# Optimization experiments

Hardware: AMD Instinct MI355X
Metric: run time of the kernel (lower is better)

Reference implementation:

```python
import jax, jax.numpy as jnp
import numpy as np

B, T, S, L, R, H, UE = 64, 256, 16, 128, 16, 256, 64


def setup_inputs() -> dict:
    key = jax.random.key(0)
    ks = jax.random.split(key, 10)
    u = jax.random.normal(ks[0], (B, T, UE), jnp.float32)
    k = 0.1 * jax.random.normal(ks[1], (B, T, L), jnp.float32)
    K = 0.1 * jax.random.normal(ks[2], (B, T, L, R), jnp.float32)
    eps_z = jax.random.normal(ks[3], (T, S, B, L), jnp.float32)
    eps_w = jax.random.normal(ks[4], (T, S, B, R), jnp.float32)
    W1 = jax.random.normal(ks[5], (L, H), jnp.float32) / np.sqrt(L).astype(np.float32)
    W2 = jax.random.normal(ks[6], (H, L), jnp.float32) / np.sqrt(H).astype(np.float32)
    m_init = jax.random.normal(ks[7], (L,), jnp.float32)
    Q_diag = jax.random.uniform(ks[8], (L,), jnp.float32, 0.1, 1.0)
    Q0_diag = jax.random.uniform(ks[9], (L,), jnp.float32, 0.5, 1.5)
    return dict(u=u, k=k, K=K, eps_z=eps_z, eps_w=eps_w, W1=W1, W2=W2,
                m_init=m_init, Q_diag=Q_diag, Q0_diag=Q0_diag, n_samples=S)


def reference(u, k, K, eps_z, eps_w, W1, W2, m_init, Q_diag, Q0_diag, n_samples):
    Bn, Tn, Ln, Rn = K.shape
    ue = u.shape[-1]
    I_r = jnp.eye(Rn, dtype=K.dtype)

    def bmv(A, x):      # A: [B,L,R], x: [...,B,R] -> [...,B,L]
        return jnp.einsum('blr,...br->...bl', A, x)

    def bmvT(A, x):     # A: [B,L,R], x: [...,B,L] -> [...,B,R]
        return jnp.einsum('blr,...bl->...br', A, x)

    def mean_fn(z):
        return z + jnp.tanh(z @ W1) @ W2

    def step_core(m, K_t, k_t, ez, ew, q_a):
        # A = I + K^T diag(q_a) K  (rank x rank)
        A = I_r + jnp.einsum('blr,l,blq->brq', K_t, q_a, K_t)
        Lc = jnp.linalg.cholesky(A)
        Linv = jax.scipy.linalg.solve_triangular(
            Lc, jnp.broadcast_to(I_r, Lc.shape), lower=True)

        def csolve(x):  # solve A y = x via Linv^T Linv x
            y = jnp.einsum('bij,...bj->...bi', Linv, x)
            return jnp.einsum('bji,...bj->...bi', Linv, y)

        # gain direction; inner shift always uses Q_diag (as in torch source)
        g = k_t - bmv(K_t, csolve(bmvT(K_t, m + Q_diag * k_t)))
        m_f = m + q_a * g
        z_p = jnp.sqrt(q_a) * ez
        z_f = m_f + z_p - bmv(K_t, csolve(bmvT(K_t, z_p) + ew))
        qp = jnp.sum(q_a * g * g, axis=-1)
        M = A - I_r  # = K^T diag(q_a) K
        tr = -jnp.einsum('bij,bjk,bik->b', Linv, M, Linv)
        logdet = 2.0 * jnp.sum(jnp.log(jnp.diagonal(Lc, axis1=-2, axis2=-1)), axis=-1)
        kl = 0.5 * (qp + tr + logdet)
        return z_f, m_f, z_p, kl

    # ---- t = 0 (uses initial covariance Q0_diag) ----
    m0 = jnp.broadcast_to(m_init, (Bn, Ln))
    m0 = m0.at[:, :ue].add(u[:, 0])
    z_f0, m_f0, z_p0, kl0 = step_core(m0, K[:, 0], k[:, 0], eps_z[0], eps_w[0], Q0_diag)

    # ---- t = 1..T-1: sequential nonlinear filter scan ----
    def scan_fn(z_prev, xs):
        u_t, k_t, K_t, ez, ew = xs
        m = mean_fn(z_prev)            # [S,B,L]
        m = m.at[..., :ue].add(u_t)    # broadcast input over samples
        z_f, m_f, z_p, kl = step_core(m, K_t, k_t, ez, ew, Q_diag)
        return z_f, (z_f, m_f.mean(axis=0), z_p, kl.mean(axis=0))

    xs = (jnp.swapaxes(u[:, 1:], 0, 1),
          jnp.swapaxes(k[:, 1:], 0, 1),
          jnp.swapaxes(K[:, 1:], 0, 1),
          eps_z[1:], eps_w[1:])
    _, (z_fs, m_fs, z_ps, kls) = jax.lax.scan(scan_fn, z_f0, xs)

    z_f = jnp.transpose(jnp.concatenate([z_f0[None], z_fs], 0), (1, 2, 0, 3))  # [S,B,T,L]
    m_f = jnp.transpose(jnp.concatenate([m_f0[None], m_fs], 0), (1, 0, 2))     # [B,T,L]
    z_p = jnp.transpose(jnp.concatenate([z_p0[None], z_ps], 0), (1, 2, 0, 3))  # [S,B,T,L]
    kl = jnp.concatenate([kl0[None], kls], 0).T                                 # [B,T]
    return z_f, m_f, z_p, kl
```

## Files before the change

kernel.cpp:

```cpp
#include <hip/hip_runtime.h>
#include <cstddef>

typedef _Float16 half8 __attribute__((ext_vector_type(8)));
typedef _Float16 half4 __attribute__((ext_vector_type(4)));
typedef float f32x4 __attribute__((ext_vector_type(4)));

#define MFMA32(A, B, C) __builtin_amdgcn_mfma_f32_16x16x32_f16(A, B, C, 0, 0, 0)
#define MFMA16(A, B, C) __builtin_amdgcn_mfma_f32_16x16x16f16(A, B, C, 0, 0, 0)

__global__ void kbp_kernel(const float* __restrict__ Kg,
                           const float* __restrict__ kg,
                           const float* __restrict__ Qd,
                           const float* __restrict__ Q0d,
                           float* __restrict__ Ainv,
                           float* __restrict__ klc,
                           float* __restrict__ Pg,
                           float* __restrict__ cg,
                           _Float16* __restrict__ Kt16) {
  int bt = blockIdx.x;
  int t = bt & 255;
  int tid = threadIdx.x;
  __shared__ float Ks[128][17];
  __shared__ float qs[128], qgl[128], kv[128];
  __shared__ float A[16][17];
  __shared__ float Lm[16][17];
  __shared__ float Li[16][17];
  __shared__ float Ai[16][17];
  __shared__ float Ps[128][17];
  __shared__ float yp[16][17];
  __shared__ float yv[16];
  __shared__ float logdet_s;

  const float* kp = Kg + (size_t)bt * 2048;
  for (int i = tid; i < 2048; i += 256) Ks[i >> 4][i & 15] = kp[i];
  if (tid < 128) {
    qs[tid] = (t == 0) ? Q0d[tid] : Qd[tid];
    qgl[tid] = Qd[tid];
    kv[tid] = kg[(size_t)bt * 128 + tid];
  }
  __syncthreads();
  {
    int r = tid >> 4, cc = tid & 15;
    float acc = (r == cc) ? 1.0f : 0.0f;
    for (int l = 0; l < 128; ++l) acc += Ks[l][r] * qs[l] * Ks[l][cc];
    A[r][cc] = acc;
  }
  __syncthreads();
  if (tid == 0) {
    float ld = 0.f;
    for (int j = 0; j < 16; ++j) {
      float d = A[j][j];
      for (int p = 0; p < j; ++p) d -= Lm[j][p] * Lm[j][p];
      d = sqrtf(d);
      Lm[j][j] = d;
      ld += logf(d);
      float inv = 1.0f / d;
      for (int i = j + 1; i < 16; ++i) {
        float s = A[i][j];
        for (int p = 0; p < j; ++p) s -= Lm[i][p] * Lm[j][p];
        Lm[i][j] = s * inv;
      }
    }
    logdet_s = 2.0f * ld;
  }
  __syncthreads();
  if (tid < 16) {
    int cc = tid;
    for (int i = 0; i < 16; ++i) {
      if (i < cc) { Li[i][cc] = 0.f; continue; }
      float s = (i == cc) ? 1.0f : 0.0f;
      for (int p = cc; p < i; ++p) s -= Lm[i][p] * Li[p][cc];
      Li[i][cc] = s / Lm[i][i];
    }
  }
  __syncthreads();
  {
    int r = tid >> 4, cc = tid & 15;
    float s = 0.f;
    for (int i = 0; i < 16; ++i) s += Li[i][r] * Li[i][cc];
    Ai[r][cc] = s;
    Ainv[(size_t)bt * 256 + tid] = s;
  }
  {
    int r = tid & 15, seg = tid >> 4;
    float s = 0.f;
    for (int l = seg * 8; l < seg * 8 + 8; ++l) s += Ks[l][r] * qgl[l] * kv[l];
    yp[seg][r] = s;
  }
  __syncthreads();
  if (tid < 16) {
    float s = 0.f;
    for (int sg = 0; sg < 16; ++sg) s += yp[sg][tid];
    yv[tid] = s;
  }
  if (tid == 0) {
    float trace = 0.f;
    for (int i = 0; i < 16; ++i) trace += Ai[i][i];
    klc[bt] = 0.5f * (trace - 16.0f + logdet_s);
  }
  {
    int l = tid >> 1, r0 = (tid & 1) * 8;
    float q = qs[l];
    float pr[8];
    for (int r = 0; r < 8; ++r) {
      float s = 0.f;
      for (int j = 0; j < 16; ++j) s += Ks[l][j] * Ai[j][r0 + r];
      pr[r] = q * s;
      Ps[l][r0 + r] = pr[r];
    }
    float* pd = Pg + (size_t)bt * 2048 + l * 16 + r0;
    f32x4 v0 = {pr[0], pr[1], pr[2], pr[3]};
    f32x4 v1 = {pr[4], pr[5], pr[6], pr[7]};
    *(f32x4*)pd = v0;
    *(f32x4*)(pd + 4) = v1;
  }
  __syncthreads();
  if (tid < 128) {
    int l = tid;
    float s = qs[l] * kv[l];
    for (int r = 0; r < 16; ++r) s -= Ps[l][r] * yv[r];
    cg[(size_t)bt * 128 + l] = s;
  }
  {
    int r = tid >> 4, l0 = (tid & 15) * 8;
    half8 v;
    for (int j = 0; j < 8; ++j) v[j] = (_Float16)Ks[l0 + j][r];
    *(half8*)(Kt16 + (size_t)bt * 2048 + r * 128 + l0) = v;
  }
}

__global__ void kc_kernel(const float* __restrict__ Kg,
                          const float* __restrict__ epsz,
                          const float* __restrict__ epsw,
                          const float* __restrict__ Qd,
                          const float* __restrict__ Q0d,
                          const float* __restrict__ Ainv,
                          float* __restrict__ out_zf,
                          float* __restrict__ out_zp,
                          int wzp) {
  int idx = blockIdx.x;
  int t = idx >> 6, b = idx & 63;
  int bt = b * 256 + t;
  __shared__ float Ks[128][16];
  __shared__ float Ai[16][16];
  __shared__ float zp[16][129];
  __shared__ float hh[16][17];
  __shared__ float ww[16][17];
  __shared__ float sq[128];
  const float* kp = Kg + (size_t)bt * 2048;
  for (int i = threadIdx.x; i < 2048; i += 256) ((float*)Ks)[i] = kp[i];
  ((float*)Ai)[threadIdx.x] = Ainv[(size_t)bt * 256 + threadIdx.x];
  const float* q = (t == 0) ? Q0d : Qd;
  if (threadIdx.x < 128) sq[threadIdx.x] = sqrtf(q[threadIdx.x]);
  __syncthreads();
  for (int i = threadIdx.x; i < 2048; i += 256) {
    int s = i >> 7, l = i & 127;
    float v = sq[l] * epsz[(((size_t)t * 16 + s) * 64 + b) * 128 + l];
    zp[s][l] = v;
    if (wzp) out_zp[(((size_t)s * 64 + b) * 256 + t) * 128 + l] = v;
  }
  __syncthreads();
  {
    int s = threadIdx.x >> 4, r = threadIdx.x & 15;
    float acc = epsw[(((size_t)t * 16 + s) * 64 + b) * 16 + r];
    for (int l = 0; l < 128; ++l) acc += Ks[l][r] * zp[s][l];
    hh[s][r] = acc;
  }
  __syncthreads();
  {
    int s = threadIdx.x >> 4, r = threadIdx.x & 15;
    float acc = 0.f;
    for (int j = 0; j < 16; ++j) acc += Ai[r][j] * hh[s][j];
    ww[s][r] = acc;
  }
  __syncthreads();
  for (int i = threadIdx.x; i < 2048; i += 256) {
    int s = i >> 7, l = i & 127;
    float acc = 0.f;
    for (int r = 0; r < 16; ++r) acc += Ks[l][r] * ww[s][r];
    out_zf[(((size_t)s * 64 + b) * 256 + t) * 128 + l] = zp[s][l] - acc;
  }
}

__global__ void kzp_kernel(const float* __restrict__ epsz,
                           const float* __restrict__ Qd,
                           const float* __restrict__ Q0d,
                           float* __restrict__ out_zp) {
  for (size_t i = (size_t)blockIdx.x * blockDim.x + threadIdx.x; i < (size_t)33554432;
       i += (size_t)gridDim.x * blockDim.x) {
    int l = (int)(i & 127);
    int t = (int)((i >> 7) & 255);
    int sb = (int)(i >> 15);
    int s = sb >> 6, b = sb & 63;
    float q = (t == 0) ? Q0d[l] : Qd[l];
    out_zp[i] = sqrtf(q) * epsz[(((size_t)t * 16 + s) * 64 + b) * 128 + l];
  }
}

__launch_bounds__(256, 1)
__global__ void kscan_kernel(const float* __restrict__ ug,
                             const float* __restrict__ W1,
                             const float* __restrict__ W2,
                             const float* __restrict__ m_init,
                             const float* __restrict__ Qd,
                             const float* __restrict__ Q0d,
                             const float* __restrict__ Pg,
                             const float* __restrict__ cg,
                             const _Float16* __restrict__ Kt16,
                             const float* __restrict__ klc,
                             float* __restrict__ out_zf,
                             float* __restrict__ out_mf,
                             float* __restrict__ out_kl) {
  const int b = blockIdx.x;
  const int tid = threadIdx.x;
  const int wv = tid >> 6;
  const int ln = tid & 63;
  const int g = ln >> 4;
  const int c = ln & 15;
  const int swz = (c & 7) << 3;

  __shared__ __align__(16) _Float16 svh[16 * 128];
  __shared__ __align__(16) _Float16 svl[16 * 128];
  __shared__ __align__(16) _Float16 hb[16 * 256];
  __shared__ float h2p[4][16][18];
  __shared__ float qpp[64];

  half8 w1f[4][4];
#pragma unroll
  for (int mt = 0; mt < 4; ++mt)
#pragma unroll
    for (int kt = 0; kt < 4; ++kt) {
      half8 v;
#pragma unroll
      for (int j = 0; j < 8; ++j)
        v[j] = (_Float16)W1[(size_t)(kt * 32 + g * 8 + j) * 256 + (wv * 64 + mt * 16 + c)];
      w1f[mt][kt] = v;
    }
  half8 w2f[2][8];
#pragma unroll
  for (int mt = 0; mt < 2; ++mt)
#pragma unroll
    for (int kt = 0; kt < 8; ++kt) {
      half8 v;
#pragma unroll
      for (int j = 0; j < 8; ++j)
        v[j] = (_Float16)W2[(size_t)(kt * 32 + g * 8 + j) * 128 + (wv * 32 + mt * 16 + c)];
      w2f[mt][kt] = v;
    }

  f32x4 qivQ[2], qivQ0[2];
#pragma unroll
  for (int mt = 0; mt < 2; ++mt) {
    int base = wv * 32 + mt * 16 + g * 4;
    f32x4 q = *(const f32x4*)&Qd[base];
    f32x4 q0 = *(const f32x4*)&Q0d[base];
#pragma unroll
    for (int r = 0; r < 4; ++r) {
      qivQ[mt][r] = 1.0f / q[r];
      qivQ0[mt][r] = 1.0f / q0[r];
    }
  }

  f32x4 zreg[2];
  f32x4 m[2];
  half4 ktfrag[2];
  f32x4 pA[2];
  f32x4 cvec[2];
  f32x4 zpcv[2];
  f32x4 ureg[2] = {};
  float klcv = 0.f;

  auto STAGE = [&](int t) {
    size_t bt = (size_t)b * 256 + t;
#pragma unroll
    for (int kt = 0; kt < 2; ++kt)
      ktfrag[kt] = *(const half4*)&Kt16[bt * 2048 + (size_t)c * 128 + wv * 32 + kt * 16 + g * 4];
#pragma unroll
    for (int mt = 0; mt < 2; ++mt) {
      pA[mt] = *(const f32x4*)&Pg[bt * 2048 + (size_t)(wv * 32 + mt * 16 + c) * 16 + g * 4];
      cvec[mt] = *(const f32x4*)&cg[bt * 128 + wv * 32 + mt * 16 + g * 4];
      zpcv[mt] = *(const f32x4*)&out_zf[(((size_t)c * 64 + b) * 256 + t) * 128 + wv * 32 + mt * 16 + g * 4];
      if (wv < 2) ureg[mt] = *(const f32x4*)&ug[bt * 64 + wv * 32 + mt * 16 + g * 4];
    }
    if (tid < 16) klcv = klc[bt];
  };

  auto MM3P = [&]() {
    f32x4 h2acc = {};
#pragma unroll
    for (int kt = 0; kt < 2; ++kt) {
      half4 mh, ml;
#pragma unroll
      for (int r = 0; r < 4; ++r) {
        float x = m[kt][r];
        _Float16 h = (_Float16)x;
        mh[r] = h;
        ml[r] = (_Float16)(x - (float)h);
      }
      h2acc = MFMA16(ktfrag[kt], mh, h2acc);
      h2acc = MFMA16(ktfrag[kt], ml, h2acc);
    }
#pragma unroll
    for (int r = 0; r < 4; ++r) h2p[wv][g * 4 + r][c] = h2acc[r];
  };

  auto PHASE_A = [&]() {
    f32x4 acc1[4] = {};
#pragma unroll
    for (int kt = 0; kt < 4; ++kt) {
      half8 zh = *(const half8*)&svh[c * 128 + ((kt * 32 + g * 8) ^ swz)];
      half8 zl = *(const half8*)&svl[c * 128 + ((kt * 32 + g * 8) ^ swz)];
#pragma unroll
      for (int mt = 0; mt < 4; ++mt) {
        acc1[mt] = MFMA32(w1f[mt][kt], zh, acc1[mt]);
        acc1[mt] = MFMA32(w1f[mt][kt], zl, acc1[mt]);
      }
    }
#pragma unroll
    for (int mt = 0; mt < 4; ++mt) {
      half4 th;
#pragma unroll
      for (int r = 0; r < 4; ++r) {
        float x = acc1[mt][r];
        float e = __expf(2.0f * x);
        th[r] = (_Float16)(1.0f - 2.0f / (e + 1.0f));
      }
      *(half4*)&hb[c * 256 + ((wv * 64 + mt * 16 + g * 4) ^ swz)] = th;
    }
  };

  auto PHASE_B = [&]() {
    f32x4 acc2[2] = {};
#pragma unroll
    for (int kt = 0; kt < 8; ++kt) {
      half8 hf = *(const half8*)&hb[c * 256 + ((kt * 32 + g * 8) ^ swz)];
#pragma unroll
      for (int mt = 0; mt < 2; ++mt) acc2[mt] = MFMA32(w2f[mt][kt], hf, acc2[mt]);
    }
#pragma unroll
    for (int mt = 0; mt < 2; ++mt) {
      m[mt] = zreg[mt] + acc2[mt];
      if (wv < 2) m[mt] += ureg[mt];
    }
    MM3P();
  };

  auto PHASE_C = [&](int t, bool q0) {
    float h2[4];
#pragma unroll
    for (int j = 0; j < 4; ++j)
      h2[j] = h2p[0][g * 4 + j][c] + h2p[1][g * 4 + j][c] + h2p[2][g * 4 + j][c] + h2p[3][g * 4 + j][c];
    half4 h2h, h2l;
#pragma unroll
    for (int j = 0; j < 4; ++j) {
      _Float16 h = (_Float16)h2[j];
      h2h[j] = h;
      h2l[j] = (_Float16)(h2[j] - (float)h);
    }
    float qpl = 0.f;
    f32x4 mfv[2];
#pragma unroll
    for (int mt = 0; mt < 2; ++mt) {
      half4 ph, pl;
#pragma unroll
      for (int r = 0; r < 4; ++r) {
        float x = pA[mt][r];
        _Float16 h = (_Float16)x;
        ph[r] = h;
        pl[r] = (_Float16)(x - (float)h);
      }
      f32x4 macc = {};
      macc = MFMA16(ph, h2h, macc);
      macc = MFMA16(ph, h2l, macc);
      macc = MFMA16(pl, h2h, macc);
      f32x4 zf4;
      f32x4 qiv = q0 ? qivQ0[mt] : qivQ[mt];
#pragma unroll
      for (int r = 0; r < 4; ++r) {
        float d = cvec[mt][r] - macc[r];
        float mf = m[mt][r] + d;
        float zf = mf + zpcv[mt][r];
        qpl += d * d * qiv[r];
        zreg[mt][r] = zf;
        zf4[r] = zf;
        mfv[mt][r] = mf;
      }
      *(f32x4*)&out_zf[(((size_t)c * 64 + b) * 256 + t) * 128 + wv * 32 + mt * 16 + g * 4] = zf4;
      half4 zh, zl;
#pragma unroll
      for (int r = 0; r < 4; ++r) {
        _Float16 h = (_Float16)zf4[r];
        zh[r] = h;
        zl[r] = (_Float16)(zf4[r] - (float)h);
      }
      *(half4*)&svh[c * 128 + ((wv * 32 + mt * 16 + g * 4) ^ swz)] = zh;
      *(half4*)&svl[c * 128 + ((wv * 32 + mt * 16 + g * 4) ^ swz)] = zl;
    }
#pragma unroll
    for (int mt = 0; mt < 2; ++mt) {
      f32x4 v = mfv[mt];
#pragma unroll
      for (int r = 0; r < 4; ++r) {
        float x = v[r];
        x += __shfl_xor(x, 1);
        x += __shfl_xor(x, 2);
        x += __shfl_xor(x, 4);
        x += __shfl_xor(x, 8);
        v[r] = x * 0.0625f;
      }
      if (c == 0)
        *(f32x4*)&out_mf[((size_t)b * 256 + t) * 128 + wv * 32 + mt * 16 + g * 4] = v;
    }
    {
      float x = qpl;
      x += __shfl_xor(x, 16);
      x += __shfl_xor(x, 32);
      if (g == 0) qpp[wv * 16 + c] = x;
    }
  };

  auto KL_FIN = [&](int t) {
    if (tid < 16) {
      float v = qpp[tid] + qpp[16 + tid] + qpp[32 + tid] + qpp[48 + tid];
      v += __shfl_xor(v, 1);
      v += __shfl_xor(v, 2);
      v += __shfl_xor(v, 4);
      v += __shfl_xor(v, 8);
      if (tid == 0) out_kl[(size_t)b * 256 + t] = 0.03125f * v + klcv;
    }
  };

  STAGE(0);
#pragma unroll
  for (int mt = 0; mt < 2; ++mt) {
    f32x4 mi = *(const f32x4*)&m_init[wv * 32 + mt * 16 + g * 4];
    if (wv < 2) mi += ureg[mt];
    m[mt] = mi;
  }
  MM3P();
  __syncthreads();
  PHASE_C(0, true);
  __syncthreads();
  KL_FIN(0);

  for (int t = 1; t < 256; ++t) {
    STAGE(t);
    PHASE_A();
    __syncthreads();
    PHASE_B();
    __syncthreads();
    PHASE_C(t, false);
    __syncthreads();
    KL_FIN(t);
  }
}

extern "C" void kernel_launch(void* const* d_in, const int* in_sizes, int n_in,
                              void* d_out, int out_size, void* d_ws, size_t ws_size,
                              hipStream_t stream) {
  (void)in_sizes; (void)n_in; (void)out_size;
  const float* u   = (const float*)d_in[0];
  const float* kk  = (const float*)d_in[1];
  const float* Kg  = (const float*)d_in[2];
  const float* epz = (const float*)d_in[3];
  const float* epw = (const float*)d_in[4];
  const float* W1  = (const float*)d_in[5];
  const float* W2  = (const float*)d_in[6];
  const float* mi  = (const float*)d_in[7];
  const float* Qd  = (const float*)d_in[8];
  const float* Q0d = (const float*)d_in[9];

  float* out_zf = (float*)d_out;
  float* out_mf = out_zf + (size_t)33554432;
  float* out_zp = out_mf + (size_t)2097152;
  float* out_kl = out_zp + (size_t)33554432;

  char* ws = (char*)d_ws;
  float* Ainv    = (float*)ws;
  float* klc     = (float*)(ws + 16777216);
  float* cg      = (float*)(ws + 16842752);
  _Float16* Kt16 = (_Float16*)(ws + 25231360);
  const size_t need_full = 226557952;
  bool fb = ws_size < need_full;
  float* Pg = fb ? out_zp : (float*)(ws + 92340224);
  int wzp = fb ? 0 : 1;

  kbp_kernel<<<16384, 256, 0, stream>>>(Kg, kk, Qd, Q0d, Ainv, klc, Pg, cg, Kt16);
  kc_kernel<<<16384, 256, 0, stream>>>(Kg, epz, epw, Qd, Q0d, Ainv, out_zf, out_zp, wzp);
  kscan_kernel<<<64, 256, 0, stream>>>(u, W1, W2, mi, Qd, Q0d, Pg, cg, Kt16, klc,
                                       out_zf, out_mf, out_kl);
  if (fb) kzp_kernel<<<2048, 256, 0, stream>>>(epz, Qd, Q0d, out_zp);
}
```

Baseline: 1.169 ms.

## Precompute K^T W2 products, restructure prep kernel per-wave, double-buffer scan staging

The prep kernel now handles four (b,t) problems per block, one per wavefront. It uses a shuffle-based Cholesky, stores P in fp16 and folds the input u into the constant term c. A new kernel precomputes R = K^T W2 in fp16, so the scan can compute K^T m as K^T z + R tanh(...) in parallel with the W2 matmul. This shortens the serial dependency chain per timestep. The scan loop is unrolled by two with double-buffered register staging of the next step's operands, and the LDS layouts are changed to a rotating swizzle. The cost is an extra precompute pass that writes a large R buffer, plus fp16 rounding of R and P.

```diff
diff --git a/kernel.cpp b/kernel.cpp
--- a/kernel.cpp
+++ b/kernel.cpp
@@ -8,124 +8,182 @@
 #define MFMA32(A, B, C) __builtin_amdgcn_mfma_f32_16x16x32_f16(A, B, C, 0, 0, 0)
 #define MFMA16(A, B, C) __builtin_amdgcn_mfma_f32_16x16x16f16(A, B, C, 0, 0, 0)
 
-__global__ void kbp_kernel(const float* __restrict__ Kg,
-                           const float* __restrict__ kg,
-                           const float* __restrict__ Qd,
-                           const float* __restrict__ Q0d,
-                           float* __restrict__ Ainv,
-                           float* __restrict__ klc,
-                           float* __restrict__ Pg,
-                           float* __restrict__ cg,
-                           _Float16* __restrict__ Kt16) {
-  int bt = blockIdx.x;
-  int t = bt & 255;
+__global__ void kprep1_kernel(const float* __restrict__ Kg,
+                              const float* __restrict__ kg,
+                              const float* __restrict__ ug,
+                              const float* __restrict__ Qd,
+                              const float* __restrict__ Q0d,
+                              float* __restrict__ Ainv,
+                              float* __restrict__ klc,
+                              _Float16* __restrict__ P16,
+                              float* __restrict__ cg) {
   int tid = threadIdx.x;
-  __shared__ float Ks[128][17];
-  __shared__ float qs[128], qgl[128], kv[128];
-  __shared__ float A[16][17];
-  __shared__ float Lm[16][17];
-  __shared__ float Li[16][17];
-  __shared__ float Ai[16][17];
-  __shared__ float Ps[128][17];
-  __shared__ float yp[16][17];
-  __shared__ float yv[16];
-  __shared__ float logdet_s;
-
-  const float* kp = Kg + (size_t)bt * 2048;
-  for (int i = tid; i < 2048; i += 256) Ks[i >> 4][i & 15] = kp[i];
-  if (tid < 128) {
-    qs[tid] = (t == 0) ? Q0d[tid] : Qd[tid];
-    qgl[tid] = Qd[tid];
-    kv[tid] = kg[(size_t)bt * 128 + tid];
-  }
-  __syncthreads();
-  {
-    int r = tid >> 4, cc = tid & 15;
-    float acc = (r == cc) ? 1.0f : 0.0f;
-    for (int l = 0; l < 128; ++l) acc += Ks[l][r] * qs[l] * Ks[l][cc];
-    A[r][cc] = acc;
-  }
-  __syncthreads();
-  if (tid == 0) {
+  int wv = tid >> 6, ln = tid & 63;
+  size_t bt = (size_t)blockIdx.x * 4 + wv;
+  int t = (int)(bt & 255);
+  __shared__ float Ks[4][128][20];
+  __shared__ float qs[4][128];
+  __shared__ float vvs[4][128];
+  __shared__ float Asm[4][16][20];
+  __shared__ float LiL[4][16][20];
+  __shared__ float AiS[4][16][20];
+  __shared__ float yps[4][4][16];
+  __shared__ float yvs[4][16];
+
+  const float* kp = Kg + bt * 2048;
+  for (int i = ln; i < 2048; i += 64) Ks[wv][i >> 4][i & 15] = kp[i];
+  for (int l = ln; l < 128; l += 64) {
+    float q = (t == 0) ? Q0d[l] : Qd[l];
+    qs[wv][l] = q;
+    float v = Qd[l] * kg[bt * 128 + l];
+    if (t > 0 && l < 64) v += ug[bt * 64 + l];
+    vvs[wv][l] = v;
+  }
+  __syncthreads();
+  {
+    int r = ln & 15, c0 = (ln >> 4) << 2;
+    float a0 = 0, a1 = 0, a2 = 0, a3 = 0;
+    for (int l = 0; l < 128; ++l) {
+      float kq = Ks[wv][l][r] * qs[wv][l];
+      const float* row = &Ks[wv][l][c0];
+      a0 += kq * row[0]; a1 += kq * row[1]; a2 += kq * row[2]; a3 += kq * row[3];
+    }
+    Asm[wv][r][c0 + 0] = a0 + ((r == c0 + 0) ? 1.f : 0.f);
+    Asm[wv][r][c0 + 1] = a1 + ((r == c0 + 1) ? 1.f : 0.f);
+    Asm[wv][r][c0 + 2] = a2 + ((r == c0 + 2) ? 1.f : 0.f);
+    Asm[wv][r][c0 + 3] = a3 + ((r == c0 + 3) ? 1.f : 0.f);
+  }
+  {
+    int r = ln & 15, seg = ln >> 4;
+    float s = 0.f;
+    for (int l = seg * 32; l < seg * 32 + 32; ++l) s += Ks[wv][l][r] * vvs[wv][l];
+    yps[wv][seg][r] = s;
+  }
+  __syncthreads();
+  if (ln < 16) {
+    int i = ln;
+    float ar[16], Lr[16];
+#pragma unroll
+    for (int j = 0; j < 16; ++j) ar[j] = Asm[wv][i][j];
     float ld = 0.f;
+#pragma unroll
     for (int j = 0; j < 16; ++j) {
-      float d = A[j][j];
-      for (int p = 0; p < j; ++p) d -= Lm[j][p] * Lm[j][p];
-      d = sqrtf(d);
-      Lm[j][j] = d;
-      ld += logf(d);
-      float inv = 1.0f / d;
-      for (int i = j + 1; i < 16; ++i) {
-        float s = A[i][j];
-        for (int p = 0; p < j; ++p) s -= Lm[i][p] * Lm[j][p];
-        Lm[i][j] = s * inv;
-      }
-    }
-    logdet_s = 2.0f * ld;
-  }
-  __syncthreads();
-  if (tid < 16) {
-    int cc = tid;
-    for (int i = 0; i < 16; ++i) {
-      if (i < cc) { Li[i][cc] = 0.f; continue; }
-      float s = (i == cc) ? 1.0f : 0.0f;
-      for (int p = cc; p < i; ++p) s -= Lm[i][p] * Li[p][cc];
-      Li[i][cc] = s / Lm[i][i];
-    }
-  }
-  __syncthreads();
-  {
-    int r = tid >> 4, cc = tid & 15;
-    float s = 0.f;
-    for (int i = 0; i < 16; ++i) s += Li[i][r] * Li[i][cc];
-    Ai[r][cc] = s;
-    Ainv[(size_t)bt * 256 + tid] = s;
-  }
-  {
-    int r = tid & 15, seg = tid >> 4;
-    float s = 0.f;
-    for (int l = seg * 8; l < seg * 8 + 8; ++l) s += Ks[l][r] * qgl[l] * kv[l];
-    yp[seg][r] = s;
-  }
-  __syncthreads();
-  if (tid < 16) {
-    float s = 0.f;
-    for (int sg = 0; sg < 16; ++sg) s += yp[sg][tid];
-    yv[tid] = s;
-  }
-  if (tid == 0) {
-    float trace = 0.f;
-    for (int i = 0; i < 16; ++i) trace += Ai[i][i];
-    klc[bt] = 0.5f * (trace - 16.0f + logdet_s);
-  }
-  {
-    int l = tid >> 1, r0 = (tid & 1) * 8;
-    float q = qs[l];
-    float pr[8];
-    for (int r = 0; r < 8; ++r) {
-      float s = 0.f;
-      for (int j = 0; j < 16; ++j) s += Ks[l][j] * Ai[j][r0 + r];
-      pr[r] = q * s;
-      Ps[l][r0 + r] = pr[r];
-    }
-    float* pd = Pg + (size_t)bt * 2048 + l * 16 + r0;
-    f32x4 v0 = {pr[0], pr[1], pr[2], pr[3]};
-    f32x4 v1 = {pr[4], pr[5], pr[6], pr[7]};
-    *(f32x4*)pd = v0;
-    *(f32x4*)(pd + 4) = v1;
-  }
-  __syncthreads();
-  if (tid < 128) {
-    int l = tid;
-    float s = qs[l] * kv[l];
-    for (int r = 0; r < 16; ++r) s -= Ps[l][r] * yv[r];
-    cg[(size_t)bt * 128 + l] = s;
-  }
-  {
-    int r = tid >> 4, l0 = (tid & 15) * 8;
-    half8 v;
-    for (int j = 0; j < 8; ++j) v[j] = (_Float16)Ks[l0 + j][r];
-    *(half8*)(Kt16 + (size_t)bt * 2048 + r * 128 + l0) = v;
+      float ajj = __shfl(ar[j], j, 64);
+      float d = sqrtf(ajj);
+      ld += __logf(d);
+      float li = ar[j] / d;
+      li = (i >= j) ? li : 0.f;
+      Lr[j] = li;
+#pragma unroll
+      for (int k2 = j; k2 < 16; ++k2) {
+        float lk = __shfl(li, k2, 64);
+        ar[k2] -= li * lk;
+      }
+    }
+    int cc = i;
+    float Lic[16];
+#pragma unroll
+    for (int ii = 0; ii < 16; ++ii) {
+      float s = (ii == cc) ? 1.f : 0.f;
+#pragma unroll
+      for (int p = 0; p < 16; ++p) {
+        if (p < ii) {
+          float Lip = __shfl(Lr[p], ii, 64);
+          s -= Lip * Lic[p];
+        }
+      }
+      float dii = __shfl(Lr[ii], ii, 64);
+      float v = s / dii;
+      Lic[ii] = (ii >= cc) ? v : 0.f;
+    }
+    float tr = 0.f;
+#pragma unroll
+    for (int ii = 0; ii < 16; ++ii) { tr += Lic[ii] * Lic[ii]; LiL[wv][cc][ii] = Lic[ii]; }
+    tr += __shfl_xor(tr, 1); tr += __shfl_xor(tr, 2);
+    tr += __shfl_xor(tr, 4); tr += __shfl_xor(tr, 8);
+    if (cc == 0) klc[bt] = 0.5f * (tr - 16.f + 2.f * ld);
+    yvs[wv][cc] = yps[wv][0][cc] + yps[wv][1][cc] + yps[wv][2][cc] + yps[wv][3][cc];
+  }
+  __syncthreads();
+  {
+    int r = ln & 15, c0 = (ln >> 4) << 2;
+    float a0 = 0, a1 = 0, a2 = 0, a3 = 0;
+    for (int ii = 0; ii < 16; ++ii) {
+      float lir = LiL[wv][r][ii];
+      a0 += lir * LiL[wv][c0 + 0][ii];
+      a1 += lir * LiL[wv][c0 + 1][ii];
+      a2 += lir * LiL[wv][c0 + 2][ii];
+      a3 += lir * LiL[wv][c0 + 3][ii];
+    }
+    AiS[wv][r][c0 + 0] = a0; AiS[wv][r][c0 + 1] = a1;
+    AiS[wv][r][c0 + 2] = a2; AiS[wv][r][c0 + 3] = a3;
+    f32x4 av = {a0, a1, a2, a3};
+    *(f32x4*)&Ainv[bt * 256 + r * 16 + c0] = av;
+  }
+  __syncthreads();
+  {
+#pragma unroll
+    for (int li = 0; li < 2; ++li) {
+      int l = ln * 2 + li;
+      f32x4 acc0 = {0,0,0,0}, acc1v = {0,0,0,0}, acc2v = {0,0,0,0}, acc3v = {0,0,0,0};
+      for (int j = 0; j < 16; ++j) {
+        float kj = Ks[wv][l][j];
+        acc0 += kj * *(const f32x4*)&AiS[wv][j][0];
+        acc1v += kj * *(const f32x4*)&AiS[wv][j][4];
+        acc2v += kj * *(const f32x4*)&AiS[wv][j][8];
+        acc3v += kj * *(const f32x4*)&AiS[wv][j][12];
+      }
+      float ql = qs[wv][l];
+      float cp = ql * kg[bt * 128 + l];
+      float pv[16];
+#pragma unroll
+      for (int e = 0; e < 4; ++e) {
+        pv[e] = ql * acc0[e]; pv[4 + e] = ql * acc1v[e];
+        pv[8 + e] = ql * acc2v[e]; pv[12 + e] = ql * acc3v[e];
+      }
+      half8 ph0, ph1;
+#pragma unroll
+      for (int r = 0; r < 16; ++r) {
+        cp -= pv[r] * yvs[wv][r];
+        if (r < 8) ph0[r] = (_Float16)pv[r]; else ph1[r - 8] = (_Float16)pv[r];
+      }
+      *(half8*)&P16[bt * 2048 + l * 16] = ph0;
+      *(half8*)&P16[bt * 2048 + l * 16 + 8] = ph1;
+      cg[bt * 128 + l] = cp;
+    }
+  }
+}
+
+__global__ void kprepR_kernel(const float* __restrict__ Kg,
+                              const float* __restrict__ W2,
+                              _Float16* __restrict__ Rg) {
+  int tid = threadIdx.x;
+  int wv = tid >> 6, ln = tid & 63;
+  int g = ln >> 4, c = ln & 15;
+  __shared__ _Float16 W2h[256 * 136];
+  for (int i = tid; i < 32768; i += 256) W2h[(i >> 7) * 136 + (i & 127)] = (_Float16)W2[i];
+  __syncthreads();
+  for (int it = 0; it < 16; ++it) {
+    size_t bt = (size_t)blockIdx.x * 16 + it;
+    half8 kA[4];
+#pragma unroll
+    for (int kt = 0; kt < 4; ++kt)
+#pragma unroll
+      for (int j = 0; j < 8; ++j)
+        kA[kt][j] = (_Float16)Kg[bt * 2048 + (size_t)(kt * 32 + g * 8 + j) * 16 + c];
+#pragma unroll
+    for (int i = 0; i < 4; ++i) {
+      int tile = wv * 4 + i;
+      f32x4 acc = {0, 0, 0, 0};
+#pragma unroll
+      for (int kt = 0; kt < 4; ++kt) {
+        half8 bf = *(const half8*)&W2h[(tile * 16 + c) * 136 + kt * 32 + g * 8];
+        acc = MFMA32(kA[kt], bf, acc);
+      }
+#pragma unroll
+      for (int r = 0; r < 4; ++r)
+        Rg[bt * 4096 + (size_t)(g * 4 + r) * 256 + tile * 16 + c] = (_Float16)acc[r];
+    }
   }
 }
 
@@ -199,14 +257,15 @@
 
 __launch_bounds__(256, 1)
 __global__ void kscan_kernel(const float* __restrict__ ug,
+                             const float* __restrict__ Kg,
                              const float* __restrict__ W1,
                              const float* __restrict__ W2,
                              const float* __restrict__ m_init,
                              const float* __restrict__ Qd,
                              const float* __restrict__ Q0d,
-                             const float* __restrict__ Pg,
+                             const _Float16* __restrict__ Pg,
                              const float* __restrict__ cg,
-                             const _Float16* __restrict__ Kt16,
+                             const _Float16* __restrict__ Rg,
                              const float* __restrict__ klc,
                              float* __restrict__ out_zf,
                              float* __restrict__ out_mf,
@@ -217,13 +276,12 @@
   const int ln = tid & 63;
   const int g = ln >> 4;
   const int c = ln & 15;
-  const int swz = (c & 7) << 3;
-
-  __shared__ __align__(16) _Float16 svh[16 * 128];
-  __shared__ __align__(16) _Float16 svl[16 * 128];
-  __shared__ __align__(16) _Float16 hb[16 * 256];
-  __shared__ float h2p[4][16][18];
-  __shared__ float qpp[64];
+
+  __shared__ __align__(16) _Float16 svh[2048];
+  __shared__ __align__(16) _Float16 svl[2048];
+  __shared__ __align__(16) _Float16 hb[4096];
+  __shared__ float h2p[4][320];
+  __shared__ float qpp[2][64];
 
   half8 w1f[4][4];
 #pragma unroll
@@ -248,211 +306,197 @@
       w2f[mt][kt] = v;
     }
 
-  f32x4 qivQ[2], qivQ0[2];
+  f32x4 qiv[2], qiv0[2];
 #pragma unroll
   for (int mt = 0; mt < 2; ++mt) {
-    int base = wv * 32 + mt * 16 + g * 4;
-    f32x4 q = *(const f32x4*)&Qd[base];
-    f32x4 q0 = *(const f32x4*)&Q0d[base];
-#pragma unroll
-    for (int r = 0; r < 4; ++r) {
-      qivQ[mt][r] = 1.0f / q[r];
-      qivQ0[mt][r] = 1.0f / q0[r];
-    }
+    f32x4 q = *(const f32x4*)&Qd[wv * 32 + mt * 16 + g * 4];
+    f32x4 q0 = *(const f32x4*)&Q0d[wv * 32 + mt * 16 + g * 4];
+#pragma unroll
+    for (int r = 0; r < 4; ++r) { qiv[mt][r] = 1.f / q[r]; qiv0[mt][r] = 1.f / q0[r]; }
   }
 
   f32x4 zreg[2];
-  f32x4 m[2];
-  half4 ktfrag[2];
-  f32x4 pA[2];
-  f32x4 cvec[2];
-  f32x4 zpcv[2];
-  f32x4 ureg[2] = {};
-  float klcv = 0.f;
-
-  auto STAGE = [&](int t) {
-    size_t bt = (size_t)b * 256 + t;
+
+  float kAf0[2][4], kAf1[2][4];
+  half4 rf0[4], rf1[4];
+  half4 pf0[2], pf1[2];
+  f32x4 cv0[2], cv1[2];
+  f32x4 zq0[2], zq1[2];
+  f32x4 ur0[2] = {}, ur1[2] = {};
+  float kv0 = 0.f, kv1 = 0.f;
+
+#define STAGE(BI, T) do { \
+    size_t bt_ = (size_t)b * 256 + (size_t)(T); \
+    const float* Kt_ = Kg + bt_ * 2048; \
+    _Pragma("unroll") for (int kt = 0; kt < 2; ++kt) \
+      _Pragma("unroll") for (int j = 0; j < 4; ++j) \
+        kAf##BI[kt][j] = Kt_[(size_t)(wv * 32 + kt * 16 + g * 4 + j) * 16 + c]; \
+    _Pragma("unroll") for (int mt = 0; mt < 4; ++mt) \
+      rf##BI[mt] = *(const half4*)&Rg[bt_ * 4096 + (size_t)c * 256 + (size_t)(wv * 64 + mt * 16 + g * 4)]; \
+    _Pragma("unroll") for (int mt = 0; mt < 2; ++mt) { \
+      pf##BI[mt] = *(const half4*)&Pg[bt_ * 2048 + (size_t)(wv * 32 + mt * 16 + c) * 16 + (size_t)(g * 4)]; \
+      cv##BI[mt] = *(const f32x4*)&cg[bt_ * 128 + wv * 32 + mt * 16 + g * 4]; \
+      zq##BI[mt] = *(const f32x4*)&out_zf[(((size_t)c * 64 + b) * 256 + (size_t)(T)) * 128 + wv * 32 + mt * 16 + g * 4]; \
+      if (wv < 2) ur##BI[mt] = *(const f32x4*)&ug[bt_ * 64 + wv * 32 + mt * 16 + g * 4]; \
+    } \
+    if (tid < 16) kv##BI = klc[bt_]; \
+  } while (0)
+
+#define PHASE_A(BI) do { \
+    half4 zbh_[2], zbl_[2]; \
+    _Pragma("unroll") for (int kt = 0; kt < 2; ++kt) \
+      _Pragma("unroll") for (int j = 0; j < 4; ++j) { \
+        float x_ = zreg[kt][j]; _Float16 h_ = (_Float16)x_; \
+        zbh_[kt][j] = h_; zbl_[kt][j] = (_Float16)(x_ - (float)h_); } \
+    f32x4 acc1_[4]; \
+    _Pragma("unroll") for (int mt = 0; mt < 4; ++mt) acc1_[mt] = (f32x4){0.f, 0.f, 0.f, 0.f}; \
+    _Pragma("unroll") for (int kt = 0; kt < 4; ++kt) { \
+      int lg_ = kt * 4 + g; \
+      int idx_ = lg_ * 128 + (((c + lg_) & 15) << 3); \
+      half8 zh8_ = *(const half8*)&svh[idx_]; \
+      half8 zl8_ = *(const half8*)&svl[idx_]; \
+      _Pragma("unroll") for (int mt = 0; mt < 4; ++mt) { \
+        acc1_[mt] = MFMA32(w1f[mt][kt], zh8_, acc1_[mt]); \
+        acc1_[mt] = MFMA32(w1f[mt][kt], zl8_, acc1_[mt]); } } \
+    half4 th_[4]; \
+    _Pragma("unroll") for (int mt = 0; mt < 4; ++mt) { \
+      _Pragma("unroll") for (int r = 0; r < 4; ++r) { \
+        float x_ = acc1_[mt][r]; \
+        float e_ = __expf(2.f * x_); \
+        th_[mt][r] = (_Float16)(1.f - 2.f / (e_ + 1.f)); } \
+      int lgw_ = wv * 8 + mt * 2 + (g >> 1); \
+      *(half4*)&hb[lgw_ * 128 + (((c + lgw_) & 15) << 3) + ((g & 1) << 2)] = th_[mt]; } \
+    f32x4 h2a_ = {0.f, 0.f, 0.f, 0.f}; \
+    _Pragma("unroll") for (int kt = 0; kt < 2; ++kt) { \
+      half4 ka_; \
+      _Pragma("unroll") for (int j = 0; j < 4; ++j) ka_[j] = (_Float16)kAf##BI[kt][j]; \
+      h2a_ = MFMA16(ka_, zbh_[kt], h2a_); \
+      h2a_ = MFMA16(ka_, zbl_[kt], h2a_); } \
+    _Pragma("unroll") for (int mt = 0; mt < 4; ++mt) h2a_ = MFMA16(rf##BI[mt], th_[mt], h2a_); \
+    *(f32x4*)&h2p[wv][c * 20 + g * 4] = h2a_; \
+  } while (0)
+
+#define EPILOG(BI, T, QIV, MV) do { \
+    f32x4 h2v_ = *(const f32x4*)&h2p[0][c * 20 + g * 4]; \
+    h2v_ += *(const f32x4*)&h2p[1][c * 20 + g * 4]; \
+    h2v_ += *(const f32x4*)&h2p[2][c * 20 + g * 4]; \
+    h2v_ += *(const f32x4*)&h2p[3][c * 20 + g * 4]; \
+    half4 h2h_, h2l_; \
+    _Pragma("unroll") for (int j = 0; j < 4; ++j) { \
+      _Float16 h_ = (_Float16)h2v_[j]; \
+      h2h_[j] = h_; h2l_[j] = (_Float16)(h2v_[j] - (float)h_); } \
+    float qpl_ = 0.f; \
+    _Pragma("unroll") for (int mt = 0; mt < 2; ++mt) { \
+      f32x4 z4_ = {0.f, 0.f, 0.f, 0.f}; \
+      f32x4 macc_ = MFMA16(pf##BI[mt], h2l_, z4_); \
+      macc_ = MFMA16(pf##BI[mt], h2h_, macc_); \
+      f32x4 dd_ = cv##BI[mt] - macc_; \
+      f32x4 mf_ = MV[mt] + dd_; \
+      f32x4 zf_ = mf_ + zq##BI[mt]; \
+      _Pragma("unroll") for (int r = 0; r < 4; ++r) qpl_ += dd_[r] * dd_[r] * QIV[mt][r]; \
+      *(f32x4*)&out_zf[(((size_t)c * 64 + b) * 256 + (size_t)(T)) * 128 + wv * 32 + mt * 16 + g * 4] = zf_; \
+      zreg[mt] = zf_; \
+      half4 zh4_, zl4_; \
+      _Pragma("unroll") for (int r = 0; r < 4; ++r) { \
+        _Float16 h_ = (_Float16)zf_[r]; \
+        zh4_[r] = h_; zl4_[r] = (_Float16)(zf_[r] - (float)h_); } \
+      int lgs_ = wv * 4 + mt * 2 + (g >> 1); \
+      int base_ = lgs_ * 128 + (((c + lgs_) & 15) << 3) + ((g & 1) << 2); \
+      *(half4*)&svh[base_] = zh4_; \
+      *(half4*)&svl[base_] = zl4_; \
+      f32x4 ms_ = mf_; \
+      _Pragma("unroll") for (int r = 0; r < 4; ++r) { \
+        float x_ = ms_[r]; \
+        x_ += __shfl_xor(x_, 1); x_ += __shfl_xor(x_, 2); \
+        x_ += __shfl_xor(x_, 4); x_ += __shfl_xor(x_, 8); \
+        ms_[r] = x_ * 0.0625f; } \
+      if (c == 0) \
+        *(f32x4*)&out_mf[((size_t)b * 256 + (size_t)(T)) * 128 + wv * 32 + mt * 16 + g * 4] = ms_; \
+    } \
+    qpl_ += __shfl_xor(qpl_, 16); \
+    qpl_ += __shfl_xor(qpl_, 32); \
+    if (g == 0) qpp[BI][wv * 16 + c] = qpl_; \
+  } while (0)
+
+#define PHASE_B(BI, T, QIV) do { \
+    f32x4 acc2_[2]; \
+    acc2_[0] = (f32x4){0.f, 0.f, 0.f, 0.f}; \
+    acc2_[1] = (f32x4){0.f, 0.f, 0.f, 0.f}; \
+    _Pragma("unroll") for (int kt = 0; kt < 8; ++kt) { \
+      int lg_ = kt * 4 + g; \
+      half8 hf_ = *(const half8*)&hb[lg_ * 128 + (((c + lg_) & 15) << 3)]; \
+      _Pragma("unroll") for (int mt = 0; mt < 2; ++mt) \
+        acc2_[mt] = MFMA32(w2f[mt][kt], hf_, acc2_[mt]); } \
+    f32x4 mv_[2]; \
+    _Pragma("unroll") for (int mt = 0; mt < 2; ++mt) { \
+      mv_[mt] = zreg[mt] + acc2_[mt]; \
+      if (wv < 2) mv_[mt] += ur##BI[mt]; } \
+    EPILOG(BI, T, QIV, mv_); \
+  } while (0)
+
+#define KL_FIN(PBI, TPREV) do { \
+    if (tid < 16) { \
+      float v_ = qpp[PBI][tid] + qpp[PBI][16 + tid] + qpp[PBI][32 + tid] + qpp[PBI][48 + tid]; \
+      v_ += __shfl_xor(v_, 1); v_ += __shfl_xor(v_, 2); \
+      v_ += __shfl_xor(v_, 4); v_ += __shfl_xor(v_, 8); \
+      if (tid == 0) out_kl[(size_t)b * 256 + (size_t)(TPREV)] = 0.03125f * v_ + kv##PBI; \
+    } \
+  } while (0)
+
+  STAGE(0, 0);
+  STAGE(1, 1);
+  {
+    f32x4 mv0[2];
+#pragma unroll
+    for (int mt = 0; mt < 2; ++mt) {
+      mv0[mt] = *(const f32x4*)&m_init[wv * 32 + mt * 16 + g * 4];
+      if (wv < 2) mv0[mt] += ur0[mt];
+    }
+    half4 zbh0[2], zbl0[2];
 #pragma unroll
     for (int kt = 0; kt < 2; ++kt)
-      ktfrag[kt] = *(const half4*)&Kt16[bt * 2048 + (size_t)c * 128 + wv * 32 + kt * 16 + g * 4];
-#pragma unroll
-    for (int mt = 0; mt < 2; ++mt) {
-      pA[mt] = *(const f32x4*)&Pg[bt * 2048 + (size_t)(wv * 32 + mt * 16 + c) * 16 + g * 4];
-      cvec[mt] = *(const f32x4*)&cg[bt * 128 + wv * 32 + mt * 16 + g * 4];
-      zpcv[mt] = *(const f32x4*)&out_zf[(((size_t)c * 64 + b) * 256 + t) * 128 + wv * 32 + mt * 16 + g * 4];
-      if (wv < 2) ureg[mt] = *(const f32x4*)&ug[bt * 64 + wv * 32 + mt * 16 + g * 4];
-    }
-    if (tid < 16) klcv = klc[bt];
-  };
-
-  auto MM3P = [&]() {
-    f32x4 h2acc = {};
+#pragma unroll
+      for (int j = 0; j < 4; ++j) {
+        float x = mv0[kt][j];
+        _Float16 h = (_Float16)x;
+        zbh0[kt][j] = h;
+        zbl0[kt][j] = (_Float16)(x - (float)h);
+      }
+    f32x4 h2a = {0.f, 0.f, 0.f, 0.f};
 #pragma unroll
     for (int kt = 0; kt < 2; ++kt) {
-      half4 mh, ml;
-#pragma unroll
-      for (int r = 0; r < 4; ++r) {
-        float x = m[kt][r];
-        _Float16 h = (_Float16)x;
-        mh[r] = h;
-        ml[r] = (_Float16)(x - (float)h);
-      }
-      h2acc = MFMA16(ktfrag[kt], mh, h2acc);
-      h2acc = MFMA16(ktfrag[kt], ml, h2acc);
-    }
-#pragma unroll
-    for (int r = 0; r < 4; ++r) h2p[wv][g * 4 + r][c] = h2acc[r];
-  };
-
-  auto PHASE_A = [&]() {
-    f32x4 acc1[4] = {};
-#pragma unroll
-    for (int kt = 0; kt < 4; ++kt) {
-      half8 zh = *(const half8*)&svh[c * 128 + ((kt * 32 + g * 8) ^ swz)];
-      half8 zl = *(const half8*)&svl[c * 128 + ((kt * 32 + g * 8) ^ swz)];
-#pragma unroll
-      for (int mt = 0; mt < 4; ++mt) {
-        acc1[mt] = MFMA32(w1f[mt][kt], zh, acc1[mt]);
-        acc1[mt] = MFMA32(w1f[mt][kt], zl, acc1[mt]);
-      }
-    }
-#pragma unroll
-    for (int mt = 0; mt < 4; ++mt) {
-      half4 th;
-#pragma unroll
-      for (int r = 0; r < 4; ++r) {
-        float x = acc1[mt][r];
-        float e = __expf(2.0f * x);
-        th[r] = (_Float16)(1.0f - 2.0f / (e + 1.0f));
-      }
-      *(half4*)&hb[c * 256 + ((wv * 64 + mt * 16 + g * 4) ^ swz)] = th;
-    }
-  };
-
-  auto PHASE_B = [&]() {
-    f32x4 acc2[2] = {};
-#pragma unroll
-    for (int kt = 0; kt < 8; ++kt) {
-      half8 hf = *(const half8*)&hb[c * 256 + ((kt * 32 + g * 8) ^ swz)];
-#pragma unroll
-      for (int mt = 0; mt < 2; ++mt) acc2[mt] = MFMA32(w2f[mt][kt], hf, acc2[mt]);
-    }
-#pragma unroll
-    for (int mt = 0; mt < 2; ++mt) {
-      m[mt] = zreg[mt] + acc2[mt];
-      if (wv < 2) m[mt] += ureg[mt];
-    }
-    MM3P();
-  };
-
-  auto PHASE_C = [&](int t, bool q0) {
-    float h2[4];
-#pragma unroll
-    for (int j = 0; j < 4; ++j)
-      h2[j] = h2p[0][g * 4 + j][c] + h2p[1][g * 4 + j][c] + h2p[2][g * 4 + j][c] + h2p[3][g * 4 + j][c];
-    half4 h2h, h2l;
-#pragma unroll
-    for (int j = 0; j < 4; ++j) {
-      _Float16 h = (_Float16)h2[j];
-      h2h[j] = h;
-      h2l[j] = (_Float16)(h2[j] - (float)h);
-    }
-    float qpl = 0.f;
-    f32x4 mfv[2];
-#pragma unroll
-    for (int mt = 0; mt < 2; ++mt) {
-      half4 ph, pl;
-#pragma unroll
-      for (int r = 0; r < 4; ++r) {
-        float x = pA[mt][r];
-        _Float16 h = (_Float16)x;
-        ph[r] = h;
-        pl[r] = (_Float16)(x - (float)h);
-      }
-      f32x4 macc = {};
-      macc = MFMA16(ph, h2h, macc);
-      macc = MFMA16(ph, h2l, macc);
-      macc = MFMA16(pl, h2h, macc);
-      f32x4 zf4;
-      f32x4 qiv = q0 ? qivQ0[mt] : qivQ[mt];
-#pragma unroll
-      for (int r = 0; r < 4; ++r) {
-        float d = cvec[mt][r] - macc[r];
-        float mf = m[mt][r] + d;
-        float zf = mf + zpcv[mt][r];
-        qpl += d * d * qiv[r];
-        zreg[mt][r] = zf;
-        zf4[r] = zf;
-        mfv[mt][r] = mf;
-      }
-      *(f32x4*)&out_zf[(((size_t)c * 64 + b) * 256 + t) * 128 + wv * 32 + mt * 16 + g * 4] = zf4;
-      half4 zh, zl;
-#pragma unroll
-      for (int r = 0; r < 4; ++r) {
-        _Float16 h = (_Float16)zf4[r];
-        zh[r] = h;
-        zl[r] = (_Float16)(zf4[r] - (float)h);
-      }
-      *(half4*)&svh[c * 128 + ((wv * 32 + mt * 16 + g * 4) ^ swz)] = zh;
-      *(half4*)&svl[c * 128 + ((wv * 32 + mt * 16 + g * 4) ^ swz)] = zl;
-    }
-#pragma unroll
-    for (int mt = 0; mt < 2; ++mt) {
-      f32x4 v = mfv[mt];
-#pragma unroll
-      for (int r = 0; r < 4; ++r) {
-        float x = v[r];
-        x += __shfl_xor(x, 1);
-        x += __shfl_xor(x, 2);
-        x += __shfl_xor(x, 4);
-        x += __shfl_xor(x, 8);
-        v[r] = x * 0.0625f;
-      }
-      if (c == 0)
-        *(f32x4*)&out_mf[((size_t)b * 256 + t) * 128 + wv * 32 + mt * 16 + g * 4] = v;
-    }
-    {
-      float x = qpl;
-      x += __shfl_xor(x, 16);
-      x += __shfl_xor(x, 32);
-      if (g == 0) qpp[wv * 16 + c] = x;
-    }
-  };
-
-  auto KL_FIN = [&](int t) {
-    if (tid < 16) {
-      float v = qpp[tid] + qpp[16 + tid] + qpp[32 + tid] + qpp[48 + tid];
-      v += __shfl_xor(v, 1);
-      v += __shfl_xor(v, 2);
-      v += __shfl_xor(v, 4);
-      v += __shfl_xor(v, 8);
-      if (tid == 0) out_kl[(size_t)b * 256 + t] = 0.03125f * v + klcv;
-    }
-  };
-
-  STAGE(0);
-#pragma unroll
-  for (int mt = 0; mt < 2; ++mt) {
-    f32x4 mi = *(const f32x4*)&m_init[wv * 32 + mt * 16 + g * 4];
-    if (wv < 2) mi += ureg[mt];
-    m[mt] = mi;
-  }
-  MM3P();
-  __syncthreads();
-  PHASE_C(0, true);
-  __syncthreads();
-  KL_FIN(0);
-
-  for (int t = 1; t < 256; ++t) {
-    STAGE(t);
-    PHASE_A();
+      half4 ka;
+#pragma unroll
+      for (int j = 0; j < 4; ++j) ka[j] = (_Float16)kAf0[kt][j];
+      h2a = MFMA16(ka, zbh0[kt], h2a);
+      h2a = MFMA16(ka, zbl0[kt], h2a);
+    }
+    *(f32x4*)&h2p[wv][c * 20 + g * 4] = h2a;
     __syncthreads();
-    PHASE_B();
+    EPILOG(0, 0, qiv0, mv0);
     __syncthreads();
-    PHASE_C(t, false);
+  }
+
+  for (int t = 1; t < 255; t += 2) {
+    KL_FIN(0, t - 1);
+    STAGE(0, t + 1);
+    PHASE_A(1);
     __syncthreads();
-    KL_FIN(t);
-  }
+    PHASE_B(1, t, qiv);
+    __syncthreads();
+    KL_FIN(1, t);
+    STAGE(1, t + 2);
+    PHASE_A(0);
+    __syncthreads();
+    PHASE_B(0, t + 1, qiv);
+    __syncthreads();
+  }
+  KL_FIN(0, 254);
+  PHASE_A(1);
+  __syncthreads();
+  PHASE_B(1, 255, qiv);
+  __syncthreads();
+  KL_FIN(1, 255);
 }
 
 extern "C" void kernel_launch(void* const* d_in, const int* in_sizes, int n_in,
@@ -479,15 +523,16 @@
   float* Ainv    = (float*)ws;
   float* klc     = (float*)(ws + 16777216);
   float* cg      = (float*)(ws + 16842752);
-  _Float16* Kt16 = (_Float16*)(ws + 25231360);
+  _Float16* P16  = (_Float16*)(ws + 25231360);
   const size_t need_full = 226557952;
   bool fb = ws_size < need_full;
-  float* Pg = fb ? out_zp : (float*)(ws + 92340224);
+  _Float16* R16 = fb ? (_Float16*)out_zp : (_Float16*)(ws + 92340224);
   int wzp = fb ? 0 : 1;
 
-  kbp_kernel<<<16384, 256, 0, stream>>>(Kg, kk, Qd, Q0d, Ainv, klc, Pg, cg, Kt16);
+  kprep1_kernel<<<4096, 256, 0, stream>>>(Kg, kk, u, Qd, Q0d, Ainv, klc, P16, cg);
+  kprepR_kernel<<<1024, 256, 0, stream>>>(Kg, W2, R16);
   kc_kernel<<<16384, 256, 0, stream>>>(Kg, epz, epw, Qd, Q0d, Ainv, out_zf, out_zp, wzp);
-  kscan_kernel<<<64, 256, 0, stream>>>(u, W1, W2, mi, Qd, Q0d, Pg, cg, Kt16, klc,
+  kscan_kernel<<<64, 256, 0, stream>>>(u, Kg, W1, W2, mi, Qd, Q0d, P16, cg, R16, klc,
                                        out_zf, out_mf, out_kl);
   if (fb) kzp_kernel<<<2048, 256, 0, stream>>>(epz, Qd, Q0d, out_zp);
 }
```

Result: slower. 1.237 ms (+5.8%).
